# Performance work log

Hardware: AMD Instinct MI355X
Metric: run time of the kernel (lower is better)

## Reference

```python
import jax, jax.numpy as jnp
import numpy as np

E = 768      # embed_size
H = 12       # num_heads inside each nn.MultiheadAttention
G = 4        # num_groups
D = E // H   # per-head dim = 64


def setup_inputs() -> dict:
    key = jax.random.key(0)
    ks = jax.random.split(key, 20)
    s = 0.02
    B, S = 2, 2048
    inp = {
        "query": jax.random.normal(ks[0], (B, S, E), jnp.float32),
        "key":   jax.random.normal(ks[1], (B, S, E), jnp.float32),
        "value": jax.random.normal(ks[2], (B, S, E), jnp.float32),
        # outer projections (query_group_proj / key_proj / value_proj)
        "Wqg": jax.random.normal(ks[3], (E, E), jnp.float32) * s,
        "bqg": jnp.zeros((E,), jnp.float32),
        "Wk":  jax.random.normal(ks[4], (E, E), jnp.float32) * s,
        "bk":  jnp.zeros((E,), jnp.float32),
        "Wv":  jax.random.normal(ks[5], (E, E), jnp.float32) * s,
        "bv":  jnp.zeros((E,), jnp.float32),
        # per-group MultiheadAttention params (in_proj split into q/k/v, out_proj)
        "Wq_in": jax.random.normal(ks[6], (G, E, E), jnp.float32) * s,
        "bq_in": jnp.zeros((G, E), jnp.float32),
        "Wk_in": jax.random.normal(ks[7], (G, E, E), jnp.float32) * s,
        "bk_in": jnp.zeros((G, E), jnp.float32),
        "Wv_in": jax.random.normal(ks[8], (G, E, E), jnp.float32) * s,
        "bv_in": jnp.zeros((G, E), jnp.float32),
        "Wout":  jax.random.normal(ks[9], (G, E, E), jnp.float32) * s,
        "bout":  jnp.zeros((G, E), jnp.float32),
    }
    return inp


def reference(query, key, value, Wqg, bqg, Wk, bk, Wv, bv,
              Wq_in, bq_in, Wk_in, bk_in, Wv_in, bv_in, Wout, bout):
    B, S, _ = query.shape
    T = S // G  # tokens per group
    scale = 1.0 / np.sqrt(D).astype(np.float32)

    # outer projections (Linear: x @ W.T + b)
    q = query @ Wqg.T + bqg                         # [B,S,E]
    k = key   @ Wk.T  + bk                          # [B,S,E]
    v = value @ Wv.T  + bv                          # [B,S,E]

    # split query tokens into G interleaved groups (view + permute in source)
    qg = q.reshape(B, T, G, E).transpose(0, 2, 1, 3)  # [B,G,T,E]

    # per-group MHA input projections (batched over groups)
    qi = jnp.einsum('bgte,gfe->bgtf', qg, Wq_in) + bq_in[None, :, None, :]
    ki = jnp.einsum('bse,gfe->bgsf', k,  Wk_in) + bk_in[None, :, None, :]
    vi = jnp.einsum('bse,gfe->bgsf', v,  Wv_in) + bv_in[None, :, None, :]

    qh = qi.reshape(B, G, T, H, D)
    kh = ki.reshape(B, G, S, H, D)
    vh = vi.reshape(B, G, S, H, D)

    scores = jnp.einsum('bgthd,bgshd->bghts', qh, kh) * scale  # [B,G,H,T,S]
    attn = jax.nn.softmax(scores, axis=-1)
    ctx = jnp.einsum('bghts,bgshd->bgthd', attn, vh).reshape(B, G, T, E)

    out_g = jnp.einsum('bgte,gfe->bgtf', ctx, Wout) + bout[None, :, None, :]  # [B,G,T,E]

    # reassemble sequence order (inverse of the grouping permutation)
    out = out_g.transpose(0, 2, 1, 3).reshape(B, S, E)
    return out
```

## Files before the change

kernel.cpp:

```cpp
#include <hip/hip_runtime.h>
#include <hip/hip_bf16.h>


typedef __attribute__((ext_vector_type(8))) short short8;
typedef __attribute__((ext_vector_type(4))) float floatx4;

static __device__ __forceinline__ short f2bf(float f) {
    unsigned u = __builtin_bit_cast(unsigned, f);
    u += 0x7FFFu + ((u >> 16) & 1u);
    return (short)(u >> 16);
}
static __device__ __forceinline__ short8 f8_to_bf8(floatx4 f0, floatx4 f1) {
    short8 s;
    s[0]=f2bf(f0[0]); s[1]=f2bf(f0[1]); s[2]=f2bf(f0[2]); s[3]=f2bf(f0[3]);
    s[4]=f2bf(f1[0]); s[5]=f2bf(f1[1]); s[6]=f2bf(f1[2]); s[7]=f2bf(f1[3]);
    return s;
}
static __device__ __forceinline__ void gload_lds16(const short* g, short* l) {
    __builtin_amdgcn_global_load_lds(
        (const __attribute__((address_space(1))) unsigned int*)g,
        (__attribute__((address_space(3))) unsigned int*)l, 16, 0, 0);
}

__global__ __launch_bounds__(256) void cast_all(
    const float* a0, const float* a1, const float* a2, const float* a3,
    const float* a4, const float* a5, const float* a6,
    const float* a7, const float* a8, const float* a9, short* dst)
{
    const long U = 589824L, M3 = 3145728L;
    const float* ptrs[10] = {a0,a1,a2,a3,a4,a5,a6,a7,a8,a9};
    const long starts[11] = {0, U, 2*U, 3*U, 7*U, 11*U, 15*U, 19*U,
                             19*U+M3, 19*U+2*M3, 19*U+3*M3};
    long i = (long)blockIdx.x * 2048 + (long)threadIdx.x * 8;
    int t = 0;
    while (t < 9 && i >= starts[t + 1]) t++;
    const float* s = ptrs[t] + (i - starts[t]);
    floatx4 f0 = *(const floatx4*)s;
    floatx4 f1 = *(const floatx4*)(s + 4);
    *(short8*)(dst + i) = f8_to_bf8(f0, f1);
}

__global__ __launch_bounds__(256) void bias_pack(
    const float* b0, const float* b1, const float* b2, const float* b3,
    const float* b4, const float* b5, const float* b6, float* dst)
{
    const int j = blockIdx.x;
    const float* src;
    if (j < 3)      src = (j == 0 ? b0 : j == 1 ? b1 : b2);
    else {
        const int jj = j - 3, w = jj >> 2, idx = jj & 3;
        const float* tb = (w == 0 ? b3 : w == 1 ? b4 : w == 2 ? b5 : b6);
        src = tb + idx * 768;
    }
#pragma unroll
    for (int r = 0; r < 3; r++)
        dst[j * 768 + r * 256 + threadIdx.x] = src[r * 256 + threadIdx.x];
}

template<int CMODE, int BIAS_ROW>
__global__ __launch_bounds__(256) void gemm_bt(
    const short* __restrict__ A, const short* __restrict__ W,
    const float* __restrict__ bias, void* __restrict__ Cv,
    int lda, long aY, long aB, long aG,
    long wY, long wB, long wG,
    long cY, long cB, long cG, int ldc,
    long bY, long bG, int nBlk)
{
    __shared__ short As[128 * 64];
    __shared__ short Bs[128 * 64];

    const int z = blockIdx.z, b = z >> 2, g = z & 3, y = blockIdx.y;
    const int bn = blockIdx.x % nBlk, bm = blockIdx.x / nBlk;
    const int tid = threadIdx.x, lane = tid & 63, w = tid >> 6;
    const int wm = w & 1, wn = w >> 1;
    const int qr = lane >> 4, lc = lane & 15, x7 = lc & 7;
    const int srow = tid >> 3, schunk = tid & 7, sx = srow & 7;

    const short* Ab = A + aY * y + aB * b + aG * g + (long)(bm * 128) * lda;
    const short* Wb = W + wY * y + wB * b + wG * g + (long)(bn * 128) * 768;
    const float* bp = bias + bY * y + bG * g;

    floatx4 acc[4][4];
#pragma unroll
    for (int mi = 0; mi < 4; mi++)
#pragma unroll
        for (int ni = 0; ni < 4; ni++) acc[mi][ni] = (floatx4){0.f, 0.f, 0.f, 0.f};

    for (int k0 = 0; k0 < 768; k0 += 64) {
        __syncthreads();
#pragma unroll
        for (int p = 0; p < 4; p++) {
            const int row = p * 32 + srow;
            const int gchunk = (schunk ^ sx) * 8;
            gload_lds16(Ab + (long)row * lda + k0 + gchunk, &As[(p * 32 + w * 8) * 64]);
            gload_lds16(Wb + (long)row * 768 + k0 + gchunk, &Bs[(p * 32 + w * 8) * 64]);
        }
        __syncthreads();
#pragma unroll
        for (int ks = 0; ks < 64; ks += 32) {
            const int c0 = (ks >> 3) + qr;
            const int slot = ((c0 ^ x7) << 3);
            short8 af[4], bfr[4];
#pragma unroll
            for (int mi = 0; mi < 4; mi++)
                af[mi] = *(const short8*)&As[(wm * 64 + mi * 16 + lc) * 64 + slot];
#pragma unroll
            for (int ni = 0; ni < 4; ni++)
                bfr[ni] = *(const short8*)&Bs[(wn * 64 + ni * 16 + lc) * 64 + slot];
#pragma unroll
            for (int mi = 0; mi < 4; mi++)
#pragma unroll
                for (int ni = 0; ni < 4; ni++)
                    acc[mi][ni] = __builtin_amdgcn_mfma_f32_16x16x32_bf16(
                        af[mi], bfr[ni], acc[mi][ni], 0, 0, 0);
        }
    }

#pragma unroll
    for (int ni = 0; ni < 4; ni++) {
        const int gcol = bn * 128 + wn * 64 + ni * 16 + lc;
        const float bcol = BIAS_ROW ? 0.f : bp[gcol];
#pragma unroll
        for (int mi = 0; mi < 4; mi++) {
#pragma unroll
            for (int r = 0; r < 4; r++) {
                const int grow = bm * 128 + wm * 64 + mi * 16 + qr * 4 + r;
                const float bb = BIAS_ROW ? bp[grow] : bcol;
                const float v = acc[mi][ni][r] + bb;
                if (CMODE == 0) {
                    short* C = (short*)Cv + cY * y + cB * b + cG * g;
                    C[(long)grow * ldc + gcol] = f2bf(v);
                } else {
                    float* C = (float*)Cv + cY * y + cB * b + cG * g;
                    C[(long)grow * ldc + gcol] = v;
                }
            }
        }
    }
}

__global__ __launch_bounds__(256) void attn_kernel(
    const short* __restrict__ qi, const short* __restrict__ ki,
    const short* __restrict__ vt, short* __restrict__ ctx)
{
    __shared__ short Kt[2][64 * 64];
    __shared__ short Vt[2][64 * 64];
    __shared__ short Ps[4][16 * 64];

    const int tid = threadIdx.x, lane = tid & 63, w = tid >> 6;
    const int qr = lane >> 4, lc = lane & 15, x7 = lc & 7;
    const int headid = blockIdx.x % 96;
    const int tile = blockIdx.x / 96;
    const int h = headid % 12, bg = headid / 12;

    const short* qp = qi + ((long)bg * 512 + tile * 64 + w * 16 + lc) * 768 + h * 64 + qr * 8;
    const short8 aq0 = *(const short8*)qp;
    const short8 aq1 = *(const short8*)(qp + 32);

    const short one = (lc == 0) ? (short)0x3F80 : (short)0;
    const short8 onesv = (short8){one, one, one, one, one, one, one, one};

    floatx4 cacc[4], lacc = (floatx4){0.f, 0.f, 0.f, 0.f};
#pragma unroll
    for (int dc = 0; dc < 4; dc++) cacc[dc] = (floatx4){0.f, 0.f, 0.f, 0.f};

    const int srow = lane >> 3, schk = lane & 7, swz = schk ^ srow;
    const short* kgb = ki + ((long)bg * 2048) * 768 + h * 64;
    const short* vgb = vt + ((long)(bg * 768 + h * 64)) * 2048;

#pragma unroll
    for (int inst = 0; inst < 2; inst++) {
        const int rk = w * 16 + inst * 8 + srow;
        gload_lds16(kgb + (long)rk * 768 + swz * 8, &Kt[0][(w * 16 + inst * 8) * 64]);
        gload_lds16(vgb + (long)rk * 2048 + swz * 8, &Vt[0][(w * 16 + inst * 8) * 64]);
    }

    for (int it = 0; it < 32; it++) {
        const int cur = it & 1;
        __syncthreads();
        if (it < 31) {
            const int nxt = cur ^ 1, s0 = (it + 1) * 64;
#pragma unroll
            for (int inst = 0; inst < 2; inst++) {
                const int rk = w * 16 + inst * 8 + srow;
                gload_lds16(kgb + (long)(s0 + rk) * 768 + swz * 8,
                            &Kt[nxt][(w * 16 + inst * 8) * 64]);
                gload_lds16(vgb + (long)rk * 2048 + s0 + swz * 8,
                            &Vt[nxt][(w * 16 + inst * 8) * 64]);
            }
        }

        const short* Kb = &Kt[cur][0];
        const short* Vb = &Vt[cur][0];

        floatx4 sv[4];
#pragma unroll
        for (int ss = 0; ss < 4; ss++) {
            const short* kr = Kb + (ss * 16 + lc) * 64;
            short8 b0 = *(const short8*)(kr + ((qr ^ x7) << 3));
            short8 b1 = *(const short8*)(kr + (((4 + qr) ^ x7) << 3));
            floatx4 t = (floatx4){0.f, 0.f, 0.f, 0.f};
            t = __builtin_amdgcn_mfma_f32_16x16x32_bf16(aq0, b0, t, 0, 0, 0);
            t = __builtin_amdgcn_mfma_f32_16x16x32_bf16(aq1, b1, t, 0, 0, 0);
            sv[ss] = t;
        }

        short* ps = &Ps[w][0];
#pragma unroll
        for (int ss = 0; ss < 4; ss++) {
            const int cch = ss * 2 + (lc >> 3);
#pragma unroll
            for (int r = 0; r < 4; r++) {
                const int m = qr * 4 + r;
                ps[m * 64 + ((cch ^ (m & 7)) << 3) + x7] =
                    f2bf(__builtin_amdgcn_exp2f(sv[ss][r] * 0.18033688f));
            }
        }
        asm volatile("s_waitcnt lgkmcnt(0)" ::: "memory");
        const short8 ap0 = *(const short8*)&ps[lc * 64 + ((qr ^ x7) << 3)];
        const short8 ap1 = *(const short8*)&ps[lc * 64 + (((4 + qr) ^ x7) << 3)];

        lacc = __builtin_amdgcn_mfma_f32_16x16x32_bf16(ap0, onesv, lacc, 0, 0, 0);
        lacc = __builtin_amdgcn_mfma_f32_16x16x32_bf16(ap1, onesv, lacc, 0, 0, 0);
#pragma unroll
        for (int dc = 0; dc < 4; dc++) {
            const short* vr = Vb + (dc * 16 + lc) * 64;
            short8 bv0 = *(const short8*)(vr + ((qr ^ x7) << 3));
            short8 bv1 = *(const short8*)(vr + (((4 + qr) ^ x7) << 3));
            cacc[dc] = __builtin_amdgcn_mfma_f32_16x16x32_bf16(ap0, bv0, cacc[dc], 0, 0, 0);
            cacc[dc] = __builtin_amdgcn_mfma_f32_16x16x32_bf16(ap1, bv1, cacc[dc], 0, 0, 0);
        }
    }

    float linv[4];
#pragma unroll
    for (int r = 0; r < 4; r++)
        linv[r] = 1.f / __shfl(lacc[r], lane & 48);
    short* cp = ctx + ((long)bg * 512 + tile * 64 + w * 16) * 768 + h * 64;
#pragma unroll
    for (int dc = 0; dc < 4; dc++)
#pragma unroll
        for (int r = 0; r < 4; r++)
            cp[(qr * 4 + r) * 768 + dc * 16 + lc] = f2bf(cacc[dc][r] * linv[r]);
}

extern "C" void kernel_launch(void* const* d_in, const int* in_sizes, int n_in,
                              void* d_out, int out_size, void* d_ws, size_t ws_size,
                              hipStream_t stream) {
    const float* query = (const float*)d_in[0];
    const float* key   = (const float*)d_in[1];
    const float* value = (const float*)d_in[2];
    const float* Wqg = (const float*)d_in[3];  const float* bqg = (const float*)d_in[4];
    const float* Wk  = (const float*)d_in[5];  const float* bk  = (const float*)d_in[6];
    const float* Wv  = (const float*)d_in[7];  const float* bv  = (const float*)d_in[8];
    const float* Wq_in = (const float*)d_in[9];  const float* bq_in = (const float*)d_in[10];
    const float* Wk_in = (const float*)d_in[11]; const float* bk_in = (const float*)d_in[12];
    const float* Wv_in = (const float*)d_in[13]; const float* bv_in = (const float*)d_in[14];
    const float* Wout  = (const float*)d_in[15]; const float* bout  = (const float*)d_in[16];
    float* out = (float*)d_out;

    const long U = 589824L;
    short* ws     = (short*)d_ws;
    short* Wbf    = ws;
    short* qbf    = ws + 11206656L;
    short* q_proj = ws + 20643840L;
    short* qiB    = ws + 30081024L;
    short* vtB    = ws + 33226752L;
    short* ctxB   = ws + 45809664L;
    short* kiB    = ws + 11206656L;
    float* PB     = (float*)(ws + 48955392L);

    dim3 blk(256);

    cast_all<<<dim3(10080), blk, 0, stream>>>(
        Wqg, Wk, Wv, Wq_in, Wk_in, Wv_in, Wout, query, key, value, Wbf);
    bias_pack<<<dim3(19), blk, 0, stream>>>(
        bqg, bk, bv, bq_in, bk_in, bv_in, bout, PB);

    gemm_bt<0, 0><<<dim3(192, 3, 1), blk, 0, stream>>>(
        qbf, Wbf, PB, q_proj, 768,
        3145728L, 0, 0,  U, 0, 0,  3145728L, 0, 0, 768,  768, 0, 6);

    gemm_bt<0, 0><<<dim3(24, 1, 8), blk, 0, stream>>>(
        q_proj, Wbf + 3 * U, PB + 3 * 768, qiB, 3072,
        0, 1572864L, 768,  0, 0, U,  0, 1572864L, 393216L, 768,  0, 768, 6);

    gemm_bt<0, 1><<<dim3(96, 1, 8), blk, 0, stream>>>(
        Wbf + 11 * U, q_proj + 6291456L, PB + 11 * 768, vtB, 768,
        0, 0, U,  0, 1572864L, 0,  0, 6291456L, 1572864L, 2048,  0, 768, 16);

    gemm_bt<0, 0><<<dim3(96, 1, 8), blk, 0, stream>>>(
        q_proj + 3145728L, Wbf + 7 * U, PB + 7 * 768, kiB, 768,
        0, 1572864L, 0,  0, 0, U,  0, 6291456L, 1572864L, 768,  0, 768, 6);

    attn_kernel<<<dim3(768), blk, 0, stream>>>(qiB, kiB, vtB, ctxB);

    gemm_bt<2, 0><<<dim3(24, 1, 8), blk, 0, stream>>>(
        ctxB, Wbf + 15 * U, PB + 15 * 768, out, 768,
        0, 1572864L, 393216L,  0, 0, U,  0, 1572864L, 768, 3072,  0, 768, 6);
}
```

Baseline: 338.5 us.

## Fuse activation cast into QKV GEMM and merge mid-stage GEMMs into one launch

```diff
diff --git a/kernel.cpp b/kernel.cpp
--- a/kernel.cpp
+++ b/kernel.cpp
@@ -6,9 +6,8 @@
 typedef __attribute__((ext_vector_type(4))) float floatx4;
 
 static __device__ __forceinline__ short f2bf(float f) {
-    unsigned u = __builtin_bit_cast(unsigned, f);
-    u += 0x7FFFu + ((u >> 16) & 1u);
-    return (short)(u >> 16);
+    __bf16 b = (__bf16)f;
+    return __builtin_bit_cast(short, b);
 }
 static __device__ __forceinline__ short8 f8_to_bf8(floatx4 f0, floatx4 f1) {
     short8 s;
@@ -22,63 +21,34 @@
         (__attribute__((address_space(3))) unsigned int*)l, 16, 0, 0);
 }
 
-__global__ __launch_bounds__(256) void cast_all(
+__global__ __launch_bounds__(256) void cast_w(
     const float* a0, const float* a1, const float* a2, const float* a3,
-    const float* a4, const float* a5, const float* a6,
-    const float* a7, const float* a8, const float* a9, short* dst)
-{
-    const long U = 589824L, M3 = 3145728L;
-    const float* ptrs[10] = {a0,a1,a2,a3,a4,a5,a6,a7,a8,a9};
-    const long starts[11] = {0, U, 2*U, 3*U, 7*U, 11*U, 15*U, 19*U,
-                             19*U+M3, 19*U+2*M3, 19*U+3*M3};
+    const float* a4, const float* a5, const float* a6, short* dst)
+{
+    const long U = 589824L;
+    const float* ptrs[7] = {a0,a1,a2,a3,a4,a5,a6};
+    const long starts[8] = {0, U, 2*U, 3*U, 7*U, 11*U, 15*U, 19*U};
     long i = (long)blockIdx.x * 2048 + (long)threadIdx.x * 8;
     int t = 0;
-    while (t < 9 && i >= starts[t + 1]) t++;
+    while (t < 6 && i >= starts[t + 1]) t++;
     const float* s = ptrs[t] + (i - starts[t]);
     floatx4 f0 = *(const floatx4*)s;
     floatx4 f1 = *(const floatx4*)(s + 4);
     *(short8*)(dst + i) = f8_to_bf8(f0, f1);
 }
 
-__global__ __launch_bounds__(256) void bias_pack(
-    const float* b0, const float* b1, const float* b2, const float* b3,
-    const float* b4, const float* b5, const float* b6, float* dst)
-{
-    const int j = blockIdx.x;
-    const float* src;
-    if (j < 3)      src = (j == 0 ? b0 : j == 1 ? b1 : b2);
-    else {
-        const int jj = j - 3, w = jj >> 2, idx = jj & 3;
-        const float* tb = (w == 0 ? b3 : w == 1 ? b4 : w == 2 ? b5 : b6);
-        src = tb + idx * 768;
-    }
-#pragma unroll
-    for (int r = 0; r < 3; r++)
-        dst[j * 768 + r * 256 + threadIdx.x] = src[r * 256 + threadIdx.x];
-}
-
-template<int CMODE, int BIAS_ROW>
-__global__ __launch_bounds__(256) void gemm_bt(
-    const short* __restrict__ A, const short* __restrict__ W,
-    const float* __restrict__ bias, void* __restrict__ Cv,
-    int lda, long aY, long aB, long aG,
-    long wY, long wB, long wG,
-    long cY, long cB, long cG, int ldc,
-    long bY, long bG, int nBlk)
-{
-    __shared__ short As[128 * 64];
-    __shared__ short Bs[128 * 64];
-
-    const int z = blockIdx.z, b = z >> 2, g = z & 3, y = blockIdx.y;
-    const int bn = blockIdx.x % nBlk, bm = blockIdx.x / nBlk;
+template<int A_IS_F32, int CMODE, int BIAS_ROW>
+static __device__ __forceinline__ void gemm_core(
+    const void* __restrict__ Av, const short* __restrict__ Wb,
+    const float* __restrict__ bp, void* __restrict__ Cv,
+    int lda, int ldc, int bm, int bn, short* As, short* Bs)
+{
     const int tid = threadIdx.x, lane = tid & 63, w = tid >> 6;
     const int wm = w & 1, wn = w >> 1;
     const int qr = lane >> 4, lc = lane & 15, x7 = lc & 7;
     const int srow = tid >> 3, schunk = tid & 7, sx = srow & 7;
 
-    const short* Ab = A + aY * y + aB * b + aG * g + (long)(bm * 128) * lda;
-    const short* Wb = W + wY * y + wB * b + wG * g + (long)(bn * 128) * 768;
-    const float* bp = bias + bY * y + bG * g;
+    const short* Wt = Wb + (long)(bn * 128) * 768;
 
     floatx4 acc[4][4];
 #pragma unroll
@@ -91,9 +61,17 @@
 #pragma unroll
         for (int p = 0; p < 4; p++) {
             const int row = p * 32 + srow;
-            const int gchunk = (schunk ^ sx) * 8;
-            gload_lds16(Ab + (long)row * lda + k0 + gchunk, &As[(p * 32 + w * 8) * 64]);
-            gload_lds16(Wb + (long)row * 768 + k0 + gchunk, &Bs[(p * 32 + w * 8) * 64]);
+            const int gch = (schunk ^ sx) * 8;
+            if (A_IS_F32) {
+                const float* ap = (const float*)Av + (long)(bm * 128 + row) * lda + k0 + gch;
+                floatx4 f0 = *(const floatx4*)ap;
+                floatx4 f1 = *(const floatx4*)(ap + 4);
+                *(short8*)&As[row * 64 + schunk * 8] = f8_to_bf8(f0, f1);
+            } else {
+                gload_lds16((const short*)Av + (long)(bm * 128 + row) * lda + k0 + gch,
+                            &As[(p * 32 + w * 8) * 64]);
+            }
+            gload_lds16(Wt + (long)row * 768 + k0 + gch, &Bs[(p * 32 + w * 8) * 64]);
         }
         __syncthreads();
 #pragma unroll
@@ -127,16 +105,63 @@
                 const int grow = bm * 128 + wm * 64 + mi * 16 + qr * 4 + r;
                 const float bb = BIAS_ROW ? bp[grow] : bcol;
                 const float v = acc[mi][ni][r] + bb;
-                if (CMODE == 0) {
-                    short* C = (short*)Cv + cY * y + cB * b + cG * g;
-                    C[(long)grow * ldc + gcol] = f2bf(v);
-                } else {
-                    float* C = (float*)Cv + cY * y + cB * b + cG * g;
-                    C[(long)grow * ldc + gcol] = v;
-                }
+                if (CMODE == 0)
+                    ((short*)Cv)[(long)grow * ldc + gcol] = f2bf(v);
+                else
+                    ((float*)Cv)[(long)grow * ldc + gcol] = v;
             }
         }
     }
+}
+
+__global__ __launch_bounds__(256) void qkv_gemm(
+    const float* q, const float* k, const float* v, const short* Wbf,
+    const float* bq, const float* bk, const float* bv, short* outp)
+{
+    __shared__ short As[128 * 64];
+    __shared__ short Bs[128 * 64];
+    const int y = blockIdx.y;
+    const float* A    = (y == 0) ? q  : (y == 1) ? k  : v;
+    const float* bias = (y == 0) ? bq : (y == 1) ? bk : bv;
+    gemm_core<1, 0, 0>(A, Wbf + (long)y * 589824, bias, outp + (long)y * 3145728,
+                       768, 768, blockIdx.x / 6, blockIdx.x % 6, As, Bs);
+}
+
+__global__ __launch_bounds__(256) void mid_gemm(
+    const short* kproj, const short* vproj, const short* qproj, const short* Wbf,
+    const float* bq_in, const float* bk_in, const float* bv_in,
+    short* kiB, short* vtB, short* qiB)
+{
+    __shared__ short As[128 * 64];
+    __shared__ short Bs[128 * 64];
+    const int z = blockIdx.z, b = z >> 2, g = z & 3;
+    const int x = blockIdx.x;
+    if (x < 96) {
+        gemm_core<0, 0, 0>(kproj + (long)b * 1572864, Wbf + (long)(7 + g) * 589824,
+                           bk_in + g * 768, kiB + (long)z * 1572864,
+                           768, 768, x / 6, x % 6, As, Bs);
+    } else if (x < 192) {
+        const int x2 = x - 96;
+        gemm_core<0, 0, 1>(Wbf + (long)(11 + g) * 589824, vproj + (long)b * 1572864,
+                           bv_in + g * 768, vtB + (long)z * 1572864,
+                           768, 2048, x2 / 16, x2 % 16, As, Bs);
+    } else {
+        const int x3 = x - 192;
+        gemm_core<0, 0, 0>(qproj + (long)b * 1572864 + g * 768, Wbf + (long)(3 + g) * 589824,
+                           bq_in + g * 768, qiB + (long)z * 393216,
+                           3072, 768, x3 / 6, x3 % 6, As, Bs);
+    }
+}
+
+__global__ __launch_bounds__(256) void out_gemm(
+    const short* ctxB, const short* Wbf, const float* bout, float* out)
+{
+    __shared__ short As[128 * 64];
+    __shared__ short Bs[128 * 64];
+    const int z = blockIdx.z, b = z >> 2, g = z & 3;
+    gemm_core<0, 2, 0>(ctxB + (long)z * 393216, Wbf + (long)(15 + g) * 589824,
+                       bout + g * 768, out + (long)b * 1572864 + g * 768,
+                       768, 3072, blockIdx.x / 6, blockIdx.x % 6, As, Bs);
 }
 
 __global__ __launch_bounds__(256) void attn_kernel(
@@ -259,43 +284,28 @@
     const float* Wout  = (const float*)d_in[15]; const float* bout  = (const float*)d_in[16];
     float* out = (float*)d_out;
 
-    const long U = 589824L;
     short* ws     = (short*)d_ws;
     short* Wbf    = ws;
-    short* qbf    = ws + 11206656L;
-    short* q_proj = ws + 20643840L;
-    short* qiB    = ws + 30081024L;
-    short* vtB    = ws + 33226752L;
-    short* ctxB   = ws + 45809664L;
-    short* kiB    = ws + 11206656L;
-    float* PB     = (float*)(ws + 48955392L);
+    short* q_proj = ws + 11206656L;
+    short* k_proj = ws + 14352384L;
+    short* v_proj = ws + 17498112L;
+    short* qiB    = ws + 20643840L;
+    short* vtB    = ws + 23789568L;
+    short* kiB    = ws + 36372480L;
+    short* ctxB   = ws + 11206656L;
 
     dim3 blk(256);
 
-    cast_all<<<dim3(10080), blk, 0, stream>>>(
-        Wqg, Wk, Wv, Wq_in, Wk_in, Wv_in, Wout, query, key, value, Wbf);
-    bias_pack<<<dim3(19), blk, 0, stream>>>(
-        bqg, bk, bv, bq_in, bk_in, bv_in, bout, PB);
-
-    gemm_bt<0, 0><<<dim3(192, 3, 1), blk, 0, stream>>>(
-        qbf, Wbf, PB, q_proj, 768,
-        3145728L, 0, 0,  U, 0, 0,  3145728L, 0, 0, 768,  768, 0, 6);
-
-    gemm_bt<0, 0><<<dim3(24, 1, 8), blk, 0, stream>>>(
-        q_proj, Wbf + 3 * U, PB + 3 * 768, qiB, 3072,
-        0, 1572864L, 768,  0, 0, U,  0, 1572864L, 393216L, 768,  0, 768, 6);
-
-    gemm_bt<0, 1><<<dim3(96, 1, 8), blk, 0, stream>>>(
-        Wbf + 11 * U, q_proj + 6291456L, PB + 11 * 768, vtB, 768,
-        0, 0, U,  0, 1572864L, 0,  0, 6291456L, 1572864L, 2048,  0, 768, 16);
-
-    gemm_bt<0, 0><<<dim3(96, 1, 8), blk, 0, stream>>>(
-        q_proj + 3145728L, Wbf + 7 * U, PB + 7 * 768, kiB, 768,
-        0, 1572864L, 0,  0, 0, U,  0, 6291456L, 1572864L, 768,  0, 768, 6);
+    cast_w<<<dim3(5472), blk, 0, stream>>>(
+        Wqg, Wk, Wv, Wq_in, Wk_in, Wv_in, Wout, Wbf);
+
+    qkv_gemm<<<dim3(192, 3, 1), blk, 0, stream>>>(
+        query, key, value, Wbf, bqg, bk, bv, q_proj);
+
+    mid_gemm<<<dim3(216, 1, 8), blk, 0, stream>>>(
+        k_proj, v_proj, q_proj, Wbf, bq_in, bk_in, bv_in, kiB, vtB, qiB);
 
     attn_kernel<<<dim3(768), blk, 0, stream>>>(qiB, kiB, vtB, ctxB);
 
-    gemm_bt<2, 0><<<dim3(24, 1, 8), blk, 0, stream>>>(
-        ctxB, Wbf + 15 * U, PB + 15 * 768, out, 768,
-        0, 1572864L, 393216L,  0, 0, U,  0, 1572864L, 768, 3072,  0, 768, 6);
-}
+    out_gemm<<<dim3(24, 1, 8), blk, 0, stream>>>(ctxB, Wbf, bout, out);
+}
```

After: 333.1 us. Within noise of the previous version (-1.6%).
